# Kernel tuning notes

Measured on AMD Instinct MI355X. Metric: run time of the kernel, lower is better.

Reference implementation:

```python
import jax, jax.numpy as jnp
import numpy as np

N_NODES = 50000
N_EDGES = 800000
NUM_FEATS = 512
NUM_CLASSES = 64
NUM_LAYERS = 4


def setup_inputs() -> dict:
    key = jax.random.key(0)
    k1, k2, k3 = jax.random.split(key, 3)
    x = jax.random.normal(k1, (N_NODES, NUM_FEATS), dtype=jnp.float32)
    # glorot init for weight [num_feats, num_classes]
    scale = jnp.sqrt(6.0 / (NUM_FEATS + NUM_CLASSES)).astype(jnp.float32)
    weight = jax.random.uniform(k2, (NUM_FEATS, NUM_CLASSES), dtype=jnp.float32,
                                minval=-scale, maxval=scale)
    edge_index = jax.random.randint(k3, (2, N_EDGES), 0, N_NODES, dtype=jnp.int64)
    return {"x": x, "weight": weight, "edge_index": edge_index}


def reference(x, weight, edge_index):
    row, col = edge_index[0], edge_index[1]  # [E], [E]
    # symmetric GCN normalization: deg^{-1/2}[row] * deg^{-1/2}[col]
    deg = jax.ops.segment_sum(jnp.ones((edge_index.shape[1],), dtype=x.dtype),
                              row, num_segments=x.shape[0])  # [N]
    deg_inv_sqrt = jnp.where(deg > 0, jax.lax.rsqrt(jnp.maximum(deg, 1e-12)), 0.0)
    norm = (deg_inv_sqrt[row] * deg_inv_sqrt[col])[:, None]  # [E, 1]

    h = x @ weight  # [N, num_classes] (dropout skipped: eval mode)
    for _ in range(NUM_LAYERS):
        # gather source features, scale by edge norm, scatter-add to destinations
        msg = norm * h[row]  # [E, num_classes]
        h = jax.ops.segment_sum(msg, col, num_segments=x.shape[0])  # [N, num_classes]
        # type_norm == 'None' -> layers_bn is identity
    return h
```

## Files before the change

kernel.cpp:

```cpp
#include <hip/hip_runtime.h>
#include <hip/hip_fp16.h>

#define NFEAT 512
#define NCLS  64
#define NNODES 50000
#define NW    (NNODES / 4)
#define NB    128
#define SLOTS 64

typedef unsigned int uint;
using short8 = __attribute__((ext_vector_type(8))) short;
using f32x4  = __attribute__((ext_vector_type(4))) float;

static __device__ __forceinline__ unsigned short f32_to_bf16_rne(float f) {
    unsigned u = __float_as_uint(f);
    unsigned r = u + 0x7FFFu + ((u >> 16) & 1u);
    return (unsigned short)(r >> 16);
}
static __device__ __forceinline__ float bf16_to_f32(unsigned short b) {
    return __uint_as_float(((unsigned)b) << 16);
}


__global__ __launch_bounds__(256) void hist_kernel(const int* __restrict__ row,
                                                   const int* __restrict__ col,
                                                   uint* __restrict__ degB,
                                                   uint* __restrict__ cntB,
                                                   int E, int CH) {
    __shared__ uint h[NW];
    int b = blockIdx.x;
    int e0 = b * CH, e1 = min(E, e0 + CH);

    for (int i = threadIdx.x; i < NW; i += 256) h[i] = 0;
    __syncthreads();
    for (int e = e0 + threadIdx.x; e < e1; e += 256) {
        int c = col[e];
        atomicAdd(&h[c >> 2], 1u << ((c & 3) * 8));
    }
    __syncthreads();
    for (int i = threadIdx.x; i < NW; i += 256) cntB[b * NW + i] = h[i];
    __syncthreads();

    for (int i = threadIdx.x; i < NW; i += 256) h[i] = 0;
    __syncthreads();
    for (int e = e0 + threadIdx.x; e < e1; e += 256) {
        int r = row[e];
        atomicAdd(&h[r >> 2], 1u << ((r & 3) * 8));
    }
    __syncthreads();
    for (int i = threadIdx.x; i < NW; i += 256) degB[b * NW + i] = h[i];
}


__global__ __launch_bounds__(256) void reduce_kernel(uint* __restrict__ cntB,
                                                     const uint* __restrict__ degB,
                                                     int* __restrict__ cntTot,
                                                     float* __restrict__ dinv) {
    int wi = blockIdx.x * 256 + threadIdx.x;
    if (wi >= NW) return;
    uint run = 0;
    for (int b = 0; b < NB; ++b) {
        uint v = cntB[b * NW + wi];
        cntB[b * NW + wi] = run;
        run += v;
    }
    int4 t = { (int)(run & 255), (int)((run >> 8) & 255),
               (int)((run >> 16) & 255), (int)((run >> 24) & 255) };
    *reinterpret_cast<int4*>(cntTot + wi * 4) = t;

    uint run2 = 0;
    for (int b = 0; b < NB; ++b) run2 += degB[b * NW + wi];
    float4 dv;
    int d0 = run2 & 255, d1 = (run2 >> 8) & 255, d2 = (run2 >> 16) & 255, d3 = run2 >> 24;
    dv.x = d0 ? rsqrtf((float)d0) : 0.0f;
    dv.y = d1 ? rsqrtf((float)d1) : 0.0f;
    dv.z = d2 ? rsqrtf((float)d2) : 0.0f;
    dv.w = d3 ? rsqrtf((float)d3) : 0.0f;
    *reinterpret_cast<float4*>(dinv + wi * 4) = dv;
}


__global__ __launch_bounds__(256) void place_kernel(const int* __restrict__ row,
                                                    const int* __restrict__ col,
                                                    const uint* __restrict__ offB,
                                                    int* __restrict__ slots,
                                                    int E, int CH) {
    __shared__ uint cur[NW];
    int b = blockIdx.x;
    int e0 = b * CH, e1 = min(E, e0 + CH);
    for (int i = threadIdx.x; i < NW; i += 256) cur[i] = offB[b * NW + i];
    __syncthreads();
    for (int e = e0 + threadIdx.x; e < e1; e += 256) {
        int c = col[e];
        uint old = atomicAdd(&cur[c >> 2], 1u << ((c & 3) * 8));
        int pos = (old >> ((c & 3) * 8)) & 255;
        if (pos < SLOTS) slots[(c << 6) + pos] = row[e];
    }
}


__global__ __launch_bounds__(256) void packw_kernel(const float* __restrict__ w,
                                                    short8* __restrict__ wp) {
    int gid = blockIdx.x * 256 + threadIdx.x;
    int lane = gid & 63;
    int F = gid >> 6;
    int s = F & 1;
    int nt = (F >> 1) & 3;
    int kk = F >> 3;
    int k0 = kk * 32 + (lane >> 4) * 8;
    int c  = nt * 16 + (lane & 15);
    short8 v;
#pragma unroll
    for (int j = 0; j < 8; ++j) {
        float x = w[(k0 + j) * NCLS + c];
        unsigned short hi = f32_to_bf16_rne(x);
        unsigned short out = hi;
        if (s) out = f32_to_bf16_rne(x - bf16_to_f32(hi));
        v[j] = (short)out;
    }
    wp[gid] = v;
}


__global__ __launch_bounds__(256, 2) void mfma_matmul_kernel(
        const float* __restrict__ x, const short8* __restrict__ wp,
        float* __restrict__ m, int N) {
    __shared__ short8 blds[2048];

    int tid = threadIdx.x;
    int wave = tid >> 6, lane = tid & 63;
    int rlo = lane & 15, khi = lane >> 4;
    int row0 = blockIdx.x * 64 + wave * 16;
    int rn = row0 + rlo; if (rn > N - 1) rn = N - 1;
    const float* xr = x + (size_t)rn * NFEAT + khi * 8;

    f32x4 acc0 = {0.f,0.f,0.f,0.f}, acc1 = {0.f,0.f,0.f,0.f};
    f32x4 acc2 = {0.f,0.f,0.f,0.f}, acc3 = {0.f,0.f,0.f,0.f};

    for (int ch = 0; ch < 4; ++ch) {
        __syncthreads();
        const short8* src = wp + ch * 2048;
        for (int i = tid; i < 2048; i += 256) blds[i] = src[i];
        __syncthreads();
#pragma unroll
        for (int kk = 0; kk < 4; ++kk) {
            int kg = ch * 128 + kk * 32;
            float4 xa = *reinterpret_cast<const float4*>(xr + kg);
            float4 xb = *reinterpret_cast<const float4*>(xr + kg + 4);
            float xs[8] = {xa.x, xa.y, xa.z, xa.w, xb.x, xb.y, xb.z, xb.w};
            short8 ahi, alo;
#pragma unroll
            for (int j = 0; j < 8; ++j) {
                unsigned short h = f32_to_bf16_rne(xs[j]);
                ahi[j] = (short)h;
                alo[j] = (short)f32_to_bf16_rne(xs[j] - bf16_to_f32(h));
            }
            const short8* fb = blds + kk * 512 + lane;
            short8 bh0 = fb[0 * 64], bl0 = fb[1 * 64];
            short8 bh1 = fb[2 * 64], bl1 = fb[3 * 64];
            short8 bh2 = fb[4 * 64], bl2 = fb[5 * 64];
            short8 bh3 = fb[6 * 64], bl3 = fb[7 * 64];
            acc0 = __builtin_amdgcn_mfma_f32_16x16x32_bf16(ahi, bh0, acc0, 0, 0, 0);
            acc1 = __builtin_amdgcn_mfma_f32_16x16x32_bf16(ahi, bh1, acc1, 0, 0, 0);
            acc2 = __builtin_amdgcn_mfma_f32_16x16x32_bf16(ahi, bh2, acc2, 0, 0, 0);
            acc3 = __builtin_amdgcn_mfma_f32_16x16x32_bf16(ahi, bh3, acc3, 0, 0, 0);
            acc0 = __builtin_amdgcn_mfma_f32_16x16x32_bf16(alo, bh0, acc0, 0, 0, 0);
            acc1 = __builtin_amdgcn_mfma_f32_16x16x32_bf16(alo, bh1, acc1, 0, 0, 0);
            acc2 = __builtin_amdgcn_mfma_f32_16x16x32_bf16(alo, bh2, acc2, 0, 0, 0);
            acc3 = __builtin_amdgcn_mfma_f32_16x16x32_bf16(alo, bh3, acc3, 0, 0, 0);
            acc0 = __builtin_amdgcn_mfma_f32_16x16x32_bf16(ahi, bl0, acc0, 0, 0, 0);
            acc1 = __builtin_amdgcn_mfma_f32_16x16x32_bf16(ahi, bl1, acc1, 0, 0, 0);
            acc2 = __builtin_amdgcn_mfma_f32_16x16x32_bf16(ahi, bl2, acc2, 0, 0, 0);
            acc3 = __builtin_amdgcn_mfma_f32_16x16x32_bf16(ahi, bl3, acc3, 0, 0, 0);
        }
    }

    int rbase = row0 + khi * 4;
#pragma unroll
    for (int j = 0; j < 4; ++j) {
        int r = rbase + j;
        if (r < N) {
            float* op = m + (size_t)r * NCLS + rlo;
            op[0]  = acc0[j];
            op[16] = acc1[j];
            op[32] = acc2[j];
            op[48] = acc3[j];
        }
    }
}


__global__ __launch_bounds__(256) void u0_kernel(const float* __restrict__ m,
                                                 const float* __restrict__ dinv,
                                                 __half* __restrict__ u, int N) {
    int n = blockIdx.x * 4 + (threadIdx.x >> 6);
    if (n >= N) return;
    int lane = threadIdx.x & 63;
    float v = m[(size_t)n * NCLS + lane] * dinv[n];
    u[(size_t)n * NCLS + lane] = __float2half(v);
}


__global__ __launch_bounds__(256) void gather_kernel(const __half* __restrict__ u,
                                                     const int* __restrict__ cntTot,
                                                     const int* __restrict__ slots,
                                                     const float* __restrict__ dinv,
                                                     __half* __restrict__ out_h,
                                                     float* __restrict__ out_f,
                                                     int N, int sq) {
    int wid = blockIdx.x * 4 + (threadIdx.x >> 6);
    if (wid >= N) return;
    int lane = threadIdx.x & 63;
    int q = lane >> 4;
    int p = lane & 15;
    int cq = cntTot[wid];
    cq = (cq < SLOTS) ? cq : SLOTS;
    const int* sl = slots + (wid << 6);

    float ax = 0.f, ay = 0.f, az = 0.f, aw = 0.f;
    float bx = 0.f, by = 0.f, bz = 0.f, bw = 0.f;
    int i = q;
    for (; i + 4 < cq; i += 8) {
        int s0 = sl[i];
        int s1 = sl[i + 4];
        uint2 d0 = *reinterpret_cast<const uint2*>(u + (size_t)s0 * NCLS + p * 4);
        uint2 d1 = *reinterpret_cast<const uint2*>(u + (size_t)s1 * NCLS + p * 4);
        float2 f0 = __half22float2(*reinterpret_cast<__half2*>(&d0.x));
        float2 f1 = __half22float2(*reinterpret_cast<__half2*>(&d0.y));
        float2 f2 = __half22float2(*reinterpret_cast<__half2*>(&d1.x));
        float2 f3 = __half22float2(*reinterpret_cast<__half2*>(&d1.y));
        ax += f0.x; ay += f0.y; az += f1.x; aw += f1.y;
        bx += f2.x; by += f2.y; bz += f3.x; bw += f3.y;
    }
    if (i < cq) {
        int s0 = sl[i];
        uint2 d0 = *reinterpret_cast<const uint2*>(u + (size_t)s0 * NCLS + p * 4);
        float2 f0 = __half22float2(*reinterpret_cast<__half2*>(&d0.x));
        float2 f1 = __half22float2(*reinterpret_cast<__half2*>(&d0.y));
        ax += f0.x; ay += f0.y; az += f1.x; aw += f1.y;
    }
    ax += bx; ay += by; az += bz; aw += bw;
#pragma unroll
    for (int off = 16; off < 64; off <<= 1) {
        ax += __shfl_xor(ax, off);
        ay += __shfl_xor(ay, off);
        az += __shfl_xor(az, off);
        aw += __shfl_xor(aw, off);
    }
    if (q == 0) {
        float sc = dinv[wid];
        if (sq) {
            sc *= sc;
            __half2 h0 = __floats2half2_rn(ax * sc, ay * sc);
            __half2 h1 = __floats2half2_rn(az * sc, aw * sc);
            uint2 d;
            d.x = *reinterpret_cast<uint*>(&h0);
            d.y = *reinterpret_cast<uint*>(&h1);
            *reinterpret_cast<uint2*>(out_h + (size_t)wid * NCLS + p * 4) = d;
        } else {
            float4 r = {ax * sc, ay * sc, az * sc, aw * sc};
            *reinterpret_cast<float4*>(out_f + (size_t)wid * NCLS + p * 4) = r;
        }
    }
}


extern "C" void kernel_launch(void* const* d_in, const int* in_sizes, int n_in,
                              void* d_out, int out_size, void* d_ws, size_t ws_size,
                              hipStream_t stream) {
    const float* x = (const float*)d_in[0];
    const float* w = (const float*)d_in[1];
    const int*   ei = (const int*)d_in[2];

    int N = in_sizes[0] / NFEAT;
    int E = in_sizes[2] / 2;
    const int* row = ei;
    const int* col = ei + E;
    float* out = (float*)d_out;

    auto align256 = [](size_t v) { return (v + 255) & ~(size_t)255; };
    char* ws = (char*)d_ws;
    size_t off = 0;
    uint* cntB   = (uint*)(ws + off);   off += align256((size_t)NB * NW * sizeof(uint));
    uint* degB   = (uint*)(ws + off);   off += align256((size_t)NB * NW * sizeof(uint));
    int* cntTot  = (int*)(ws + off);    off += align256((size_t)NNODES * sizeof(int));
    float* dinv  = (float*)(ws + off);  off += align256((size_t)NNODES * sizeof(float));
    short8* wp   = (short8*)(ws + off); off += align256((size_t)8192 * sizeof(short8));
    int* slots   = (int*)(ws + off);    off += align256((size_t)NNODES * SLOTS * sizeof(int));
    __half* uA   = (__half*)(ws + off); off += align256((size_t)NNODES * NCLS * sizeof(__half));
    __half* uB   = (__half*)(ws + off); off += align256((size_t)NNODES * NCLS * sizeof(__half));

    int CH = (E + NB - 1) / NB;

    packw_kernel<<<32, 256, 0, stream>>>(w, wp);
    hist_kernel<<<NB, 256, 0, stream>>>(row, col, degB, cntB, E, CH);
    reduce_kernel<<<(NW + 255) / 256, 256, 0, stream>>>(cntB, degB, cntTot, dinv);
    place_kernel<<<NB, 256, 0, stream>>>(row, col, cntB, slots, E, CH);

    mfma_matmul_kernel<<<(N + 63) / 64, 256, 0, stream>>>(x, wp, out, N);

    int ngrid = (N + 3) / 4;
    u0_kernel<<<ngrid, 256, 0, stream>>>(out, dinv, uA, N);

    gather_kernel<<<ngrid, 256, 0, stream>>>(uA, cntTot, slots, dinv, uB, nullptr, N, 1);
    gather_kernel<<<ngrid, 256, 0, stream>>>(uB, cntTot, slots, dinv, uA, nullptr, N, 1);
    gather_kernel<<<ngrid, 256, 0, stream>>>(uA, cntTot, slots, dinv, uB, nullptr, N, 1);
    gather_kernel<<<ngrid, 256, 0, stream>>>(uB, cntTot, slots, dinv, nullptr, out, N, 0);
}
```

Before: 192.4 us.

## Fuse preprocessing kernels, merge place with matmul, widen gather loads

Merges the histogram and weight-packing kernels into one launch that counts col and row in a single pass over edges using a doubled shared buffer. It also merges edge placement with the MFMA matmul via block-index partitioning, folds the u0 scaling into the matmul epilogue, and splits the reduce work across twice as many threads. The number of histogram blocks is doubled, and the gather kernel switches to 16-byte loads with 8 lanes per row. Together these cut launch count and intermediate traffic, at the cost of higher shared-memory use per block, which may lower occupancy, and a longer serial scan in reduce.

```diff
diff --git a/kernel.cpp b/kernel.cpp
--- a/kernel.cpp
+++ b/kernel.cpp
@@ -5,7 +5,7 @@
 #define NCLS  64
 #define NNODES 50000
 #define NW    (NNODES / 4)
-#define NB    128
+#define NB    256
 #define SLOTS 64
 
 typedef unsigned int uint;
@@ -22,86 +22,32 @@
 }
 
 
-__global__ __launch_bounds__(256) void hist_kernel(const int* __restrict__ row,
-                                                   const int* __restrict__ col,
-                                                   uint* __restrict__ degB,
-                                                   uint* __restrict__ cntB,
-                                                   int E, int CH) {
-    __shared__ uint h[NW];
+__global__ __launch_bounds__(256) void hist_packw_kernel(
+        const int* __restrict__ row, const int* __restrict__ col,
+        const float* __restrict__ w,
+        uint* __restrict__ degB, uint* __restrict__ cntB,
+        short8* __restrict__ wp, int E, int CH) {
+    __shared__ __align__(16) uint h[2 * NW];
     int b = blockIdx.x;
-    int e0 = b * CH, e1 = min(E, e0 + CH);
-
-    for (int i = threadIdx.x; i < NW; i += 256) h[i] = 0;
-    __syncthreads();
-    for (int e = e0 + threadIdx.x; e < e1; e += 256) {
-        int c = col[e];
-        atomicAdd(&h[c >> 2], 1u << ((c & 3) * 8));
-    }
-    __syncthreads();
-    for (int i = threadIdx.x; i < NW; i += 256) cntB[b * NW + i] = h[i];
-    __syncthreads();
-
-    for (int i = threadIdx.x; i < NW; i += 256) h[i] = 0;
-    __syncthreads();
-    for (int e = e0 + threadIdx.x; e < e1; e += 256) {
-        int r = row[e];
-        atomicAdd(&h[r >> 2], 1u << ((r & 3) * 8));
-    }
-    __syncthreads();
-    for (int i = threadIdx.x; i < NW; i += 256) degB[b * NW + i] = h[i];
-}
-
-
-__global__ __launch_bounds__(256) void reduce_kernel(uint* __restrict__ cntB,
-                                                     const uint* __restrict__ degB,
-                                                     int* __restrict__ cntTot,
-                                                     float* __restrict__ dinv) {
-    int wi = blockIdx.x * 256 + threadIdx.x;
-    if (wi >= NW) return;
-    uint run = 0;
-    for (int b = 0; b < NB; ++b) {
-        uint v = cntB[b * NW + wi];
-        cntB[b * NW + wi] = run;
-        run += v;
-    }
-    int4 t = { (int)(run & 255), (int)((run >> 8) & 255),
-               (int)((run >> 16) & 255), (int)((run >> 24) & 255) };
-    *reinterpret_cast<int4*>(cntTot + wi * 4) = t;
-
-    uint run2 = 0;
-    for (int b = 0; b < NB; ++b) run2 += degB[b * NW + wi];
-    float4 dv;
-    int d0 = run2 & 255, d1 = (run2 >> 8) & 255, d2 = (run2 >> 16) & 255, d3 = run2 >> 24;
-    dv.x = d0 ? rsqrtf((float)d0) : 0.0f;
-    dv.y = d1 ? rsqrtf((float)d1) : 0.0f;
-    dv.z = d2 ? rsqrtf((float)d2) : 0.0f;
-    dv.w = d3 ? rsqrtf((float)d3) : 0.0f;
-    *reinterpret_cast<float4*>(dinv + wi * 4) = dv;
-}
-
-
-__global__ __launch_bounds__(256) void place_kernel(const int* __restrict__ row,
-                                                    const int* __restrict__ col,
-                                                    const uint* __restrict__ offB,
-                                                    int* __restrict__ slots,
-                                                    int E, int CH) {
-    __shared__ uint cur[NW];
-    int b = blockIdx.x;
-    int e0 = b * CH, e1 = min(E, e0 + CH);
-    for (int i = threadIdx.x; i < NW; i += 256) cur[i] = offB[b * NW + i];
-    __syncthreads();
-    for (int e = e0 + threadIdx.x; e < e1; e += 256) {
-        int c = col[e];
-        uint old = atomicAdd(&cur[c >> 2], 1u << ((c & 3) * 8));
-        int pos = (old >> ((c & 3) * 8)) & 255;
-        if (pos < SLOTS) slots[(c << 6) + pos] = row[e];
-    }
-}
-
-
-__global__ __launch_bounds__(256) void packw_kernel(const float* __restrict__ w,
-                                                    short8* __restrict__ wp) {
-    int gid = blockIdx.x * 256 + threadIdx.x;
+    if (b < NB) {
+        for (int i = threadIdx.x; i < 2 * NW; i += 256) h[i] = 0;
+        __syncthreads();
+        int e0 = b * CH, e1 = min(E, e0 + CH);
+        for (int e = e0 + threadIdx.x; e < e1; e += 256) {
+            int c = col[e], r = row[e];
+            atomicAdd(&h[c >> 2], 1u << ((c & 3) * 8));
+            atomicAdd(&h[NW + (r >> 2)], 1u << ((r & 3) * 8));
+        }
+        __syncthreads();
+        uint4* cb = reinterpret_cast<uint4*>(cntB + (size_t)b * NW);
+        uint4* db = reinterpret_cast<uint4*>(degB + (size_t)b * NW);
+        const uint4* c4 = reinterpret_cast<const uint4*>(h);
+        const uint4* d4 = reinterpret_cast<const uint4*>(h + NW);
+        for (int i = threadIdx.x; i < NW / 4; i += 256) cb[i] = c4[i];
+        for (int i = threadIdx.x; i < NW / 4; i += 256) db[i] = d4[i];
+        return;
+    }
+    int gid = (b - NB) * 256 + threadIdx.x;
     int lane = gid & 63;
     int F = gid >> 6;
     int s = F & 1;
@@ -112,25 +58,79 @@
     short8 v;
 #pragma unroll
     for (int j = 0; j < 8; ++j) {
-        float x = w[(k0 + j) * NCLS + c];
-        unsigned short hi = f32_to_bf16_rne(x);
-        unsigned short out = hi;
-        if (s) out = f32_to_bf16_rne(x - bf16_to_f32(hi));
-        v[j] = (short)out;
+        float xv = w[(k0 + j) * NCLS + c];
+        unsigned short hi = f32_to_bf16_rne(xv);
+        unsigned short outv = hi;
+        if (s) outv = f32_to_bf16_rne(xv - bf16_to_f32(hi));
+        v[j] = (short)outv;
     }
     wp[gid] = v;
 }
 
 
-__global__ __launch_bounds__(256, 2) void mfma_matmul_kernel(
+__global__ __launch_bounds__(256) void reduce_kernel(uint* __restrict__ cntB,
+                                                     const uint* __restrict__ degB,
+                                                     int* __restrict__ cntTot,
+                                                     float* __restrict__ dinv) {
+    int gid = blockIdx.x * 256 + threadIdx.x;
+    if (gid < NW) {
+        int wi = gid;
+        uint run = 0;
+#pragma unroll 8
+        for (int b = 0; b < NB; ++b) {
+            uint v = cntB[(size_t)b * NW + wi];
+            cntB[(size_t)b * NW + wi] = run;
+            run += v;
+        }
+        int4 t = { (int)(run & 255), (int)((run >> 8) & 255),
+                   (int)((run >> 16) & 255), (int)(run >> 24) };
+        *reinterpret_cast<int4*>(cntTot + wi * 4) = t;
+    } else if (gid < 2 * NW) {
+        int wi = gid - NW;
+        uint run = 0;
+#pragma unroll 8
+        for (int b = 0; b < NB; ++b) run += degB[(size_t)b * NW + wi];
+        int d0 = run & 255, d1 = (run >> 8) & 255, d2 = (run >> 16) & 255, d3 = run >> 24;
+        float4 dv;
+        dv.x = d0 ? rsqrtf((float)d0) : 0.0f;
+        dv.y = d1 ? rsqrtf((float)d1) : 0.0f;
+        dv.z = d2 ? rsqrtf((float)d2) : 0.0f;
+        dv.w = d3 ? rsqrtf((float)d3) : 0.0f;
+        *reinterpret_cast<float4*>(dinv + wi * 4) = dv;
+    }
+}
+
+
+__global__ __launch_bounds__(256, 2) void place_matmul_kernel(
+        const int* __restrict__ row, const int* __restrict__ col,
+        const uint* __restrict__ offB, int* __restrict__ slots,
         const float* __restrict__ x, const short8* __restrict__ wp,
-        float* __restrict__ m, int N) {
-    __shared__ short8 blds[2048];
-
+        const float* __restrict__ dinv, __half* __restrict__ u0,
+        int N, int E, int CH) {
+    __shared__ __align__(16) uint sh[NW];
+    int b = blockIdx.x;
+
+    if (b < NB) {
+        uint4* c4 = reinterpret_cast<uint4*>(sh);
+        const uint4* o4 = reinterpret_cast<const uint4*>(offB + (size_t)b * NW);
+        for (int i = threadIdx.x; i < NW / 4; i += 256) c4[i] = o4[i];
+        __syncthreads();
+        int e0 = b * CH, e1 = min(E, e0 + CH);
+        for (int e = e0 + threadIdx.x; e < e1; e += 256) {
+            int c = col[e];
+            uint old = atomicAdd(&sh[c >> 2], 1u << ((c & 3) * 8));
+            int pos = (old >> ((c & 3) * 8)) & 255;
+            if (pos < SLOTS) slots[(c << 6) + pos] = row[e];
+        }
+        return;
+    }
+
+    short8* blds = reinterpret_cast<short8*>(sh);
+    int tile = b - NB;
     int tid = threadIdx.x;
     int wave = tid >> 6, lane = tid & 63;
     int rlo = lane & 15, khi = lane >> 4;
-    int row0 = blockIdx.x * 64 + wave * 16;
+    int row0 = tile * 64 + wave * 16;
     int rn = row0 + rlo; if (rn > N - 1) rn = N - 1;
     const float* xr = x + (size_t)rn * NFEAT + khi * 8;
 
@@ -151,9 +151,9 @@
             short8 ahi, alo;
 #pragma unroll
             for (int j = 0; j < 8; ++j) {
-                unsigned short h = f32_to_bf16_rne(xs[j]);
-                ahi[j] = (short)h;
-                alo[j] = (short)f32_to_bf16_rne(xs[j] - bf16_to_f32(h));
+                unsigned short hh = f32_to_bf16_rne(xs[j]);
+                ahi[j] = (short)hh;
+                alo[j] = (short)f32_to_bf16_rne(xs[j] - bf16_to_f32(hh));
             }
             const short8* fb = blds + kk * 512 + lane;
             short8 bh0 = fb[0 * 64], bl0 = fb[1 * 64];
@@ -180,24 +180,14 @@
     for (int j = 0; j < 4; ++j) {
         int r = rbase + j;
         if (r < N) {
-            float* op = m + (size_t)r * NCLS + rlo;
-            op[0]  = acc0[j];
-            op[16] = acc1[j];
-            op[32] = acc2[j];
-            op[48] = acc3[j];
-        }
-    }
-}
-
-
-__global__ __launch_bounds__(256) void u0_kernel(const float* __restrict__ m,
-                                                 const float* __restrict__ dinv,
-                                                 __half* __restrict__ u, int N) {
-    int n = blockIdx.x * 4 + (threadIdx.x >> 6);
-    if (n >= N) return;
-    int lane = threadIdx.x & 63;
-    float v = m[(size_t)n * NCLS + lane] * dinv[n];
-    u[(size_t)n * NCLS + lane] = __float2half(v);
+            float dn = dinv[r];
+            __half* op = u0 + ((size_t)r << 6) + rlo;
+            op[0]  = __float2half(acc0[j] * dn);
+            op[16] = __float2half(acc1[j] * dn);
+            op[32] = __float2half(acc2[j] * dn);
+            op[48] = __float2half(acc3[j] * dn);
+        }
+    }
 }
 
 
@@ -211,55 +201,72 @@
     int wid = blockIdx.x * 4 + (threadIdx.x >> 6);
     if (wid >= N) return;
     int lane = threadIdx.x & 63;
-    int q = lane >> 4;
-    int p = lane & 15;
+    int q = lane >> 3;
+    int p = lane & 7;
     int cq = cntTot[wid];
     cq = (cq < SLOTS) ? cq : SLOTS;
     const int* sl = slots + (wid << 6);
 
-    float ax = 0.f, ay = 0.f, az = 0.f, aw = 0.f;
-    float bx = 0.f, by = 0.f, bz = 0.f, bw = 0.f;
+    float a0=0.f,a1=0.f,a2=0.f,a3=0.f,a4=0.f,a5=0.f,a6=0.f,a7=0.f;
+    float b0=0.f,b1=0.f,b2=0.f,b3=0.f,b4=0.f,b5=0.f,b6=0.f,b7=0.f;
     int i = q;
-    for (; i + 4 < cq; i += 8) {
+    for (; i + 8 < cq; i += 16) {
         int s0 = sl[i];
-        int s1 = sl[i + 4];
-        uint2 d0 = *reinterpret_cast<const uint2*>(u + (size_t)s0 * NCLS + p * 4);
-        uint2 d1 = *reinterpret_cast<const uint2*>(u + (size_t)s1 * NCLS + p * 4);
+        int s1 = sl[i + 8];
+        uint4 d0 = *reinterpret_cast<const uint4*>(u + ((size_t)s0 << 6) + p * 8);
+        uint4 d1 = *reinterpret_cast<const uint4*>(u + ((size_t)s1 << 6) + p * 8);
         float2 f0 = __half22float2(*reinterpret_cast<__half2*>(&d0.x));
         float2 f1 = __half22float2(*reinterpret_cast<__half2*>(&d0.y));
-        float2 f2 = __half22float2(*reinterpret_cast<__half2*>(&d1.x));
-        float2 f3 = __half22float2(*reinterpret_cast<__half2*>(&d1.y));
-        ax += f0.x; ay += f0.y; az += f1.x; aw += f1.y;
-        bx += f2.x; by += f2.y; bz += f3.x; bw += f3.y;
+        float2 f2 = __half22float2(*reinterpret_cast<__half2*>(&d0.z));
+        float2 f3 = __half22float2(*reinterpret_cast<__half2*>(&d0.w));
+        a0 += f0.x; a1 += f0.y; a2 += f1.x; a3 += f1.y;
+        a4 += f2.x; a5 += f2.y; a6 += f3.x; a7 += f3.y;
+        float2 g0 = __half22float2(*reinterpret_cast<__half2*>(&d1.x));
+        float2 g1 = __half22float2(*reinterpret_cast<__half2*>(&d1.y));
+        float2 g2 = __half22float2(*reinterpret_cast<__half2*>(&d1.z));
+        float2 g3 = __half22float2(*reinterpret_cast<__half2*>(&d1.w));
+        b0 += g0.x; b1 += g0.y; b2 += g1.x; b3 += g1.y;
+        b4 += g2.x; b5 += g2.y; b6 += g3.x; b7 += g3.y;
     }
     if (i < cq) {
         int s0 = sl[i];
-        uint2 d0 = *reinterpret_cast<const uint2*>(u + (size_t)s0 * NCLS + p * 4);
+        uint4 d0 = *reinterpret_cast<const uint4*>(u + ((size_t)s0 << 6) + p * 8);
         float2 f0 = __half22float2(*reinterpret_cast<__half2*>(&d0.x));
         float2 f1 = __half22float2(*reinterpret_cast<__half2*>(&d0.y));
-        ax += f0.x; ay += f0.y; az += f1.x; aw += f1.y;
-    }
-    ax += bx; ay += by; az += bz; aw += bw;
-#pragma unroll
-    for (int off = 16; off < 64; off <<= 1) {
-        ax += __shfl_xor(ax, off);
-        ay += __shfl_xor(ay, off);
-        az += __shfl_xor(az, off);
-        aw += __shfl_xor(aw, off);
+        float2 f2 = __half22float2(*reinterpret_cast<__half2*>(&d0.z));
+        float2 f3 = __half22float2(*reinterpret_cast<__half2*>(&d0.w));
+        a0 += f0.x; a1 += f0.y; a2 += f1.x; a3 += f1.y;
+        a4 += f2.x; a5 += f2.y; a6 += f3.x; a7 += f3.y;
+    }
+    a0 += b0; a1 += b1; a2 += b2; a3 += b3;
+    a4 += b4; a5 += b5; a6 += b6; a7 += b7;
+#pragma unroll
+    for (int off = 8; off < 64; off <<= 1) {
+        a0 += __shfl_xor(a0, off); a1 += __shfl_xor(a1, off);
+        a2 += __shfl_xor(a2, off); a3 += __shfl_xor(a3, off);
+        a4 += __shfl_xor(a4, off); a5 += __shfl_xor(a5, off);
+        a6 += __shfl_xor(a6, off); a7 += __shfl_xor(a7, off);
     }
     if (q == 0) {
         float sc = dinv[wid];
         if (sq) {
             sc *= sc;
-            __half2 h0 = __floats2half2_rn(ax * sc, ay * sc);
-            __half2 h1 = __floats2half2_rn(az * sc, aw * sc);
-            uint2 d;
+            __half2 h0 = __floats2half2_rn(a0 * sc, a1 * sc);
+            __half2 h1 = __floats2half2_rn(a2 * sc, a3 * sc);
+            __half2 h2 = __floats2half2_rn(a4 * sc, a5 * sc);
+            __half2 h3 = __floats2half2_rn(a6 * sc, a7 * sc);
+            uint4 d;
             d.x = *reinterpret_cast<uint*>(&h0);
             d.y = *reinterpret_cast<uint*>(&h1);
-            *reinterpret_cast<uint2*>(out_h + (size_t)wid * NCLS + p * 4) = d;
+            d.z = *reinterpret_cast<uint*>(&h2);
+            d.w = *reinterpret_cast<uint*>(&h3);
+            *reinterpret_cast<uint4*>(out_h + ((size_t)wid << 6) + p * 8) = d;
         } else {
-            float4 r = {ax * sc, ay * sc, az * sc, aw * sc};
-            *reinterpret_cast<float4*>(out_f + (size_t)wid * NCLS + p * 4) = r;
+            float4 r0 = {a0 * sc, a1 * sc, a2 * sc, a3 * sc};
+            float4 r1 = {a4 * sc, a5 * sc, a6 * sc, a7 * sc};
+            float4* op = reinterpret_cast<float4*>(out_f + ((size_t)wid << 6) + p * 8);
+            op[0] = r0;
+            op[1] = r1;
         }
     }
 }
@@ -292,16 +299,13 @@
 
     int CH = (E + NB - 1) / NB;
 
-    packw_kernel<<<32, 256, 0, stream>>>(w, wp);
-    hist_kernel<<<NB, 256, 0, stream>>>(row, col, degB, cntB, E, CH);
-    reduce_kernel<<<(NW + 255) / 256, 256, 0, stream>>>(cntB, degB, cntTot, dinv);
-    place_kernel<<<NB, 256, 0, stream>>>(row, col, cntB, slots, E, CH);
-
-    mfma_matmul_kernel<<<(N + 63) / 64, 256, 0, stream>>>(x, wp, out, N);
+    hist_packw_kernel<<<NB + 32, 256, 0, stream>>>(row, col, w, degB, cntB, wp, E, CH);
+    reduce_kernel<<<(2 * NW + 255) / 256, 256, 0, stream>>>(cntB, degB, cntTot, dinv);
+    int nmm = (N + 63) / 64;
+    place_matmul_kernel<<<NB + nmm, 256, 0, stream>>>(row, col, cntB, slots,
+                                                      x, wp, dinv, uA, N, E, CH);
 
     int ngrid = (N + 3) / 4;
-    u0_kernel<<<ngrid, 256, 0, stream>>>(out, dinv, uA, N);
-
     gather_kernel<<<ngrid, 256, 0, stream>>>(uA, cntTot, slots, dinv, uB, nullptr, N, 1);
     gather_kernel<<<ngrid, 256, 0, stream>>>(uB, cntTot, slots, dinv, uA, nullptr, N, 1);
     gather_kernel<<<ngrid, 256, 0, stream>>>(uA, cntTot, slots, dinv, uB, nullptr, N, 1);
```

After: 165.7 us. 13.9% less time.
